# Optimization experiments

Hardware: AMD Instinct MI355X
Metric: run time of the kernel (lower is better)

The kernel has to match this reference:

```python
import jax, jax.numpy as jnp
import numpy as np

B, CIN, F, H, W = 4, 256, 128, 64, 64
EPS = 1e-5

def _conv1x1(x, Wm, b):
    # x: [B,C,H,W], Wm: [O,C] (1x1 conv kernel), b: [O]
    return jnp.einsum('bchw,oc->bohw', x, Wm) + b[None, :, None, None]

def setup_inputs() -> dict:
    key = jax.random.key(0)
    ks = jax.random.split(key, 11)
    s_in = 1.0 / np.sqrt(CIN)
    s_f = 1.0 / np.sqrt(F)
    return {
        'x':    jax.random.normal(ks[0], (B, CIN, H, W), jnp.float32),
        'Wg':   jax.random.normal(ks[1], (F, CIN), jnp.float32) * s_in,
        'bg':   jax.random.normal(ks[2], (F,), jnp.float32) * s_in,
        'Wt':   jax.random.normal(ks[3], (F, CIN), jnp.float32) * s_in,
        'bt':   jax.random.normal(ks[4], (F,), jnp.float32) * s_in,
        'Wp':   jax.random.normal(ks[5], (F, CIN), jnp.float32) * s_in,
        'bp':   jax.random.normal(ks[6], (F,), jnp.float32) * s_in,
        'Wz':   jax.random.normal(ks[7], (CIN, F), jnp.float32) * s_f,
        'bz':   jax.random.normal(ks[8], (CIN,), jnp.float32) * s_f,
        'ln_w': jax.random.normal(ks[9], (CIN, H, W), jnp.float32) * 0.1,
        'ln_b': jax.random.normal(ks[10], (CIN, H, W), jnp.float32) * 0.1,
    }

def reference(x, Wg, bg, Wt, bt, Wp, bp, Wz, bz, ln_w, ln_b):
    b, _, h, w = x.shape
    n = h * w
    # 1x1 conv projections
    g = _conv1x1(x, Wg, bg).reshape(b, F, n).transpose(0, 2, 1)      # [B,N,F]
    theta = _conv1x1(x, Wt, bt).reshape(b, F, n).transpose(0, 2, 1)  # [B,N,F]
    phi = _conv1x1(x, Wp, bp).reshape(b, F, n)                        # [B,F,N]
    # embedded-Gaussian affinity + softmax attention
    f = jnp.einsum('bnf,bfm->bnm', theta, phi)                        # [B,N,N]
    attn = jax.nn.softmax(f, axis=-1)
    y = jnp.einsum('bnm,bmf->bnf', attn, g)                           # [B,N,F]
    y = y.transpose(0, 2, 1).reshape(b, F, h, w)                      # [B,F,H,W]
    # output projection
    z = _conv1x1(y, Wz, bz)                                           # [B,CIN,H,W]
    # LayerNorm over (C,H,W) per sample, affine params shaped [C,H,W]
    mu = jnp.mean(z, axis=(1, 2, 3), keepdims=True)
    var = jnp.var(z, axis=(1, 2, 3), keepdims=True)
    z = (z - mu) * jax.lax.rsqrt(var + EPS)
    z = z * ln_w[None] + ln_b[None]
    return z + x
```

## Files before the change

kernel.cpp:

```cpp
#include <hip/hip_runtime.h>
#include <stdint.h>

#define CIN 256
#define FDIM 128
#define NSP 4096
#define EPS 1e-5f

typedef __attribute__((ext_vector_type(8))) short short8;
typedef __attribute__((ext_vector_type(4))) float f32x4;
typedef __attribute__((ext_vector_type(16))) float f32x16;

__device__ __forceinline__ short f2bf(float f) {
  union { float f; uint32_t u; } v; v.f = f;
  uint32_t r = v.u + 0x7fffu + ((v.u >> 16) & 1u);
  return (short)(r >> 16);
}
__device__ __forceinline__ float bf2f(short h) {
  union { uint32_t u; float f; } v; v.u = ((uint32_t)(uint16_t)h) << 16;
  return v.f;
}

__global__ void prep_weights(const float* __restrict__ Wg, const float* __restrict__ Wt,
                             const float* __restrict__ Wp, const float* __restrict__ Wz,
                             short* __restrict__ Wbf, short* __restrict__ Wzbf) {
  int idx = blockIdx.x * 256 + threadIdx.x;
  if (idx < 384 * 256) {
    int row = idx >> 8, col = idx & 255;
    float v;
    if (row < 128)       v = Wt[row * 256 + col];
    else if (row < 256)  v = Wp[(row - 128) * 256 + col];
    else                 v = Wg[(row - 256) * 256 + col];
    Wbf[idx] = f2bf(v);
  } else {
    int j = idx - 384 * 256;
    if (j < 256 * 128) Wzbf[j] = f2bf(Wz[j]);
  }
}

__global__ void prep_xT(const float* __restrict__ x, short* __restrict__ xT) {
  __shared__ float tile[32][33];
  int b = blockIdx.z, c0 = blockIdx.y * 32, n0 = blockIdx.x * 32;
  int r = threadIdx.x >> 5, c = threadIdx.x & 31;
  const float* xb = x + (size_t)b * CIN * NSP;
#pragma unroll
  for (int k = 0; k < 4; k++)
    tile[r + 8 * k][c] = xb[(size_t)(c0 + r + 8 * k) * NSP + n0 + c];
  __syncthreads();
  short* xTb = xT + (size_t)b * NSP * CIN;
#pragma unroll
  for (int k = 0; k < 4; k++)
    xTb[(size_t)(n0 + r + 8 * k) * CIN + c0 + c] = f2bf(tile[c][r + 8 * k]);
}

__global__ void __launch_bounds__(256)
proj_kernel(const short* __restrict__ xT, const short* __restrict__ Wbf,
            const float* __restrict__ bt, const float* __restrict__ bp,
            const float* __restrict__ bg,
            short* __restrict__ theta, short* __restrict__ Kb, short* __restrict__ gT) {
  __shared__ short lds[5120];
  int bx = blockIdx.x;
  int b = bx >> 7;
  int n0 = (bx & 127) << 5;
  int p = blockIdx.y;
  int t = threadIdx.x, w = t >> 6, lane = t & 63, l15 = lane & 15, quad = lane >> 4;

  const short* arow = xT + (size_t)(b * NSP + n0 + (w & 1) * 16 + l15) * CIN;
  short8 a[8];
#pragma unroll
  for (int s = 0; s < 8; s++) a[s] = *(const short8*)(arow + s * 32 + quad * 8);

  const short* Wsrc = Wbf + p * 128 * 256;
  f32x4 zero = {0.f, 0.f, 0.f, 0.f};
  f32x4 acc[4];
#pragma unroll
  for (int i = 0; i < 4; i++) acc[i] = zero;

#pragma unroll
  for (int s = 0; s < 8; s++) {
#pragma unroll
    for (int ft = 0; ft < 4; ft++) {
      int ftg = (w >> 1) * 4 + ft;
      short8 bfr = *(const short8*)(Wsrc + (ftg * 16 + l15) * 256 + s * 32 + quad * 8);
      acc[ft] = __builtin_amdgcn_mfma_f32_16x16x32_bf16(a[s], bfr, acc[ft], 0, 0, 0);
    }
  }

  const float* bias = (p == 0) ? bt : (p == 1) ? bp : bg;
  if (p < 2) {
#pragma unroll
    for (int ft = 0; ft < 4; ft++) {
      int ftg = (w >> 1) * 4 + ft;
      float bv = bias[ftg * 16 + l15];
#pragma unroll
      for (int rr = 0; rr < 4; rr++) {
        int n = (w & 1) * 16 + quad * 4 + rr;
        lds[n * 136 + ftg * 16 + l15] = f2bf(acc[ft][rr] + bv);
      }
    }
    __syncthreads();
    short* dst = ((p == 0) ? theta : Kb) + (size_t)(b * NSP + n0) * FDIM;
#pragma unroll
    for (int i = 0; i < 2; i++) {
      int flat = t + 256 * i;
      int row = flat >> 4, ch = flat & 15;
      *(short8*)(dst + (size_t)row * FDIM + ch * 8) = *(const short8*)(lds + row * 136 + ch * 8);
    }
  } else {
#pragma unroll
    for (int ft = 0; ft < 4; ft++) {
      int ftg = (w >> 1) * 4 + ft;
      float bv = bias[ftg * 16 + l15];
#pragma unroll
      for (int rr = 0; rr < 4; rr++) {
        int n = (w & 1) * 16 + quad * 4 + rr;
        lds[(ftg * 16 + l15) * 40 + n] = f2bf(acc[ft][rr] + bv);
      }
    }
    __syncthreads();
    short* dst = gT + (size_t)b * FDIM * NSP + n0;
#pragma unroll
    for (int i = 0; i < 2; i++) {
      int flat = t + 256 * i;
      int f = flat >> 2, c = flat & 3;
      *(short8*)(dst + (size_t)f * NSP + c * 8) = *(const short8*)(lds + f * 40 + c * 8);
    }
  }
}

__global__ void __launch_bounds__(256, 2)
flash_kernel(const short* __restrict__ thetab, const short* __restrict__ Kb,
             const short* __restrict__ gT, short* __restrict__ opart,
             float* __restrict__ lpart) {
  __shared__ __attribute__((aligned(16))) char smem[66048];
  short* KldsA = (short*)smem;
  short* KldsB = (short*)(smem + 8704);
  short* VtA   = (short*)(smem + 17408);
  short* VtB   = (short*)(smem + 27648);
  float* Om    = (float*)smem;
  float* lsm   = (float*)(smem + 65536);

  const int bx = blockIdx.x;
  const int b  = bx >> 7;
  const int r  = bx & 127;
  const int q0 = (r >> 2) << 7;
  const int kc = r & 3;
  const int t = threadIdx.x, w = t >> 6, lane = t & 63;
  const int l31 = lane & 31, h = lane >> 5;
  const int qw = q0 + (w & 1) * 64;

  const short* Qsrc = thetab + (size_t)b * NSP * FDIM;
  const short* Ksrc = Kb + (size_t)b * NSP * FDIM;
  const short* Vsrc = gT + (size_t)b * FDIM * NSP;

  short8 qf0[8], qf1[8];
#pragma unroll
  for (int s = 0; s < 8; s++) {
    qf0[s] = *(const short8*)(Qsrc + (size_t)(qw + l31) * FDIM + s * 16 + h * 8);
    qf1[s] = *(const short8*)(Qsrc + (size_t)(qw + 32 + l31) * FDIM + s * 16 + h * 8);
  }

  f32x16 O0[4], O1[4];
#pragma unroll
  for (int i = 0; i < 4; i++) {
#pragma unroll
    for (int j = 0; j < 16; j++) { O0[i][j] = 0.f; O1[i][j] = 0.f; }
  }
  float lsum0 = 0.f, lsum1 = 0.f;

  const int kA0 = kc << 10;
  for (int j0 = 0; j0 < 512; j0 += 32) {
    __syncthreads();
    int kA = kA0 + j0, kB = kA + 512;
#pragma unroll
    for (int rep = 0; rep < 2; rep++) {
      int flat = t + 256 * rep;
      int row = flat >> 4, c = flat & 15;
      *(short8*)(KldsA + row * 136 + c * 8) =
          *(const short8*)(Ksrc + (size_t)(kA + row) * FDIM + c * 8);
      *(short8*)(KldsB + row * 136 + c * 8) =
          *(const short8*)(Ksrc + (size_t)(kB + row) * FDIM + c * 8);
      int f = flat >> 2, c2 = flat & 3;
      *(short8*)(VtA + f * 40 + c2 * 8) =
          *(const short8*)(Vsrc + (size_t)f * NSP + kA + c2 * 8);
      *(short8*)(VtB + f * 40 + c2 * 8) =
          *(const short8*)(Vsrc + (size_t)f * NSP + kB + c2 * 8);
    }
    __syncthreads();
    const short* Kl = (w & 2) ? KldsB : KldsA;
    const short* Vl = (w & 2) ? VtB : VtA;

    f32x16 S0, S1;
#pragma unroll
    for (int j = 0; j < 16; j++) { S0[j] = 0.f; S1[j] = 0.f; }
#pragma unroll
    for (int s = 0; s < 8; s++) {
      short8 ak = *(const short8*)(Kl + l31 * 136 + s * 16 + h * 8);
      S0 = __builtin_amdgcn_mfma_f32_32x32x16_bf16(ak, qf0[s], S0, 0, 0, 0);
      S1 = __builtin_amdgcn_mfma_f32_32x32x16_bf16(ak, qf1[s], S1, 0, 0, 0);
    }

    short8 Af0[2], Af1[2];
#pragma unroll
    for (int qb = 0; qb < 2; qb++) {
      float p[16];
      float ls = 0.f;
#pragma unroll
      for (int i = 0; i < 16; i++) {
        p[i] = __expf(qb ? S1[i] : S0[i]);
        ls += p[i];
      }
      if (qb) lsum1 += ls; else lsum0 += ls;
#pragma unroll
      for (int tt = 0; tt < 2; tt++) {
        const int rb = tt * 8;
        short8 af;
#pragma unroll
        for (int rr = 0; rr < 4; rr++) {
          float qv = h ? p[rb + rr] : p[rb + 4 + rr];
          float wv = __shfl_xor(qv, 32, 64);
          float e0 = h ? wv : p[rb + rr];
          float e1 = h ? p[rb + 4 + rr] : wv;
          af[rr] = f2bf(e0);
          af[4 + rr] = f2bf(e1);
        }
        if (qb) Af1[tt] = af; else Af0[tt] = af;
      }
    }

#pragma unroll
    for (int ft = 0; ft < 4; ft++) {
#pragma unroll
      for (int tt = 0; tt < 2; tt++) {
        short8 bv = *(const short8*)(Vl + (ft * 32 + l31) * 40 + tt * 16 + h * 8);
        O0[ft] = __builtin_amdgcn_mfma_f32_32x32x16_bf16(Af0[tt], bv, O0[ft], 0, 0, 0);
        O1[ft] = __builtin_amdgcn_mfma_f32_32x32x16_bf16(Af1[tt], bv, O1[ft], 0, 0, 0);
      }
    }
  }

  lsum0 += __shfl_xor(lsum0, 32, 64);
  lsum1 += __shfl_xor(lsum1, 32, 64);

  __syncthreads();
  if (w >= 2) {
    float* dst = Om + (size_t)(w - 2) * 8192;
#pragma unroll
    for (int qb = 0; qb < 2; qb++) {
#pragma unroll
      for (int ft = 0; ft < 4; ft++) {
#pragma unroll
        for (int reg = 0; reg < 16; reg++) {
          int rowq = qb * 32 + (reg & 3) + 8 * (reg >> 2) + 4 * h;
          dst[rowq * 128 + ft * 32 + l31] = qb ? O1[ft][reg] : O0[ft][reg];
        }
      }
    }
    if (h == 0) {
      lsm[(w - 2) * 64 + l31] = lsum0;
      lsm[(w - 2) * 64 + 32 + l31] = lsum1;
    }
  }
  __syncthreads();
  if (w < 2) {
    const float* src = Om + (size_t)w * 8192;
    short* od = opart + ((size_t)(kc * 4 + b) * NSP + qw) * FDIM;
#pragma unroll
    for (int qb = 0; qb < 2; qb++) {
#pragma unroll
      for (int ft = 0; ft < 4; ft++) {
#pragma unroll
        for (int reg = 0; reg < 16; reg++) {
          int rowq = qb * 32 + (reg & 3) + 8 * (reg >> 2) + 4 * h;
          float v = (qb ? O1[ft][reg] : O0[ft][reg]) + src[rowq * 128 + ft * 32 + l31];
          od[(size_t)rowq * FDIM + ft * 32 + l31] = f2bf(v);
        }
      }
    }
    if (h == 0) {
      size_t lb = (size_t)(kc * 4 + b) * NSP + qw;
      lpart[lb + l31] = lsum0 + lsm[w * 64 + l31];
      lpart[lb + 32 + l31] = lsum1 + lsm[w * 64 + 32 + l31];
    }
  }
}

__global__ void __launch_bounds__(256)
zproj_kernel(const short* __restrict__ opart, const float* __restrict__ lpart,
             const short* __restrict__ Wzbf, const float* __restrict__ bz,
             short* __restrict__ zb, float* __restrict__ psums) {
  __shared__ short ldsT[128 * 40];
  __shared__ float wsum[4][2];
  int bx = blockIdx.x;
  int b = bx >> 7;
  int n0 = (bx & 127) << 5;
  int ch0 = blockIdx.y * 128;
  int t = threadIdx.x, w = t >> 6, lane = t & 63, l15 = lane & 15, quad = lane >> 4;

  int row = n0 + (w & 1) * 16 + l15;
  float L = 0.f;
#pragma unroll
  for (int kcc = 0; kcc < 4; kcc++) L += lpart[(size_t)(kcc * 4 + b) * NSP + row];
  float inv = 1.0f / L;

  short8 a[4];
#pragma unroll
  for (int s = 0; s < 4; s++) {
    float accv[8] = {0, 0, 0, 0, 0, 0, 0, 0};
#pragma unroll
    for (int kcc = 0; kcc < 4; kcc++) {
      short8 v = *(const short8*)(opart + ((size_t)(kcc * 4 + b) * NSP + row) * FDIM + s * 32 + quad * 8);
#pragma unroll
      for (int j = 0; j < 8; j++) accv[j] += bf2f(v[j]);
    }
    short8 av;
#pragma unroll
    for (int j = 0; j < 8; j++) av[j] = f2bf(accv[j] * inv);
    a[s] = av;
  }

  f32x4 zero = {0.f, 0.f, 0.f, 0.f};
  f32x4 acc[4];
#pragma unroll
  for (int i = 0; i < 4; i++) acc[i] = zero;
#pragma unroll
  for (int s = 0; s < 4; s++) {
#pragma unroll
    for (int ct = 0; ct < 4; ct++) {
      int co = ch0 + (w >> 1) * 64 + ct * 16 + l15;
      short8 bfr = *(const short8*)(Wzbf + (size_t)co * FDIM + s * 32 + quad * 8);
      acc[ct] = __builtin_amdgcn_mfma_f32_16x16x32_bf16(a[s], bfr, acc[ct], 0, 0, 0);
    }
  }

  float s1 = 0.0f, s2 = 0.0f;
#pragma unroll
  for (int ct = 0; ct < 4; ct++) {
    int cg = (w >> 1) * 64 + ct * 16 + l15;
    float bv = bz[ch0 + cg];
#pragma unroll
    for (int rr = 0; rr < 4; rr++) {
      float v = acc[ct][rr] + bv;
      s1 += v; s2 += v * v;
      ldsT[cg * 40 + (w & 1) * 16 + quad * 4 + rr] = f2bf(v);
    }
  }
#pragma unroll
  for (int off = 32; off >= 1; off >>= 1) {
    s1 += __shfl_xor(s1, off, 64);
    s2 += __shfl_xor(s2, off, 64);
  }
  if (lane == 0) { wsum[w][0] = s1; wsum[w][1] = s2; }
  __syncthreads();
  if (t == 0) {
    int bid = blockIdx.y * 512 + bx;
    psums[bid * 2] = wsum[0][0] + wsum[1][0] + wsum[2][0] + wsum[3][0];
    psums[bid * 2 + 1] = wsum[0][1] + wsum[1][1] + wsum[2][1] + wsum[3][1];
  }
  short* dst = zb + (size_t)b * CIN * NSP + (size_t)ch0 * NSP + n0;
#pragma unroll
  for (int i = 0; i < 2; i++) {
    int flat = t + 256 * i;
    int c = flat >> 2, ch = flat & 3;
    *(short8*)(dst + (size_t)c * NSP + ch * 8) = *(const short8*)(ldsT + c * 40 + ch * 8);
  }
}

__global__ void reduce_sums(const float* __restrict__ psums, float* __restrict__ sums) {
  __shared__ float red[8];
  int t = threadIdx.x;
  if (t < 8) red[t] = 0.f;
  __syncthreads();
  for (int i = t; i < 1024; i += 256) {
    int b = (i & 511) >> 7;
    atomicAdd(&red[b * 2], psums[i * 2]);
    atomicAdd(&red[b * 2 + 1], psums[i * 2 + 1]);
  }
  __syncthreads();
  if (t < 8) sums[t] = red[t];
}

__global__ void __launch_bounds__(256)
finalize_kernel(const short* __restrict__ zbuf, const float* __restrict__ x,
                const float* __restrict__ lnw, const float* __restrict__ lnb,
                const float* __restrict__ sums, float* __restrict__ out) {
  int gid = blockIdx.x * 256 + threadIdx.x;
  size_t e0 = (size_t)gid * 8;
  int b = (int)(e0 >> 20);
  size_t ib = e0 & ((size_t)(1u << 20) - 1);
  float mean = sums[b * 2] * (1.0f / 1048576.0f);
  float var = sums[b * 2 + 1] * (1.0f / 1048576.0f) - mean * mean;
  float rs = rsqrtf(var + EPS);
  short8 zv = *(const short8*)(zbuf + e0);
#pragma unroll
  for (int k = 0; k < 8; k++) {
    float z = bf2f(zv[k]);
    out[e0 + k] = (z - mean) * rs * lnw[ib + k] + lnb[ib + k] + x[e0 + k];
  }
}

extern "C" void kernel_launch(void* const* d_in, const int* in_sizes, int n_in,
                              void* d_out, int out_size, void* d_ws, size_t ws_size,
                              hipStream_t stream) {
  const float* x   = (const float*)d_in[0];
  const float* Wg  = (const float*)d_in[1];
  const float* bg  = (const float*)d_in[2];
  const float* Wt  = (const float*)d_in[3];
  const float* bt  = (const float*)d_in[4];
  const float* Wp  = (const float*)d_in[5];
  const float* bp  = (const float*)d_in[6];
  const float* Wz  = (const float*)d_in[7];
  const float* bz  = (const float*)d_in[8];
  const float* lnw = (const float*)d_in[9];
  const float* lnb = (const float*)d_in[10];
  float* out = (float*)d_out;

  char* ws = (char*)d_ws;
  short* Wbf    = (short*)(ws);
  short* Wzbf   = (short*)(ws + 196608);
  short* xT     = (short*)(ws + 262144);
  short* opart  = (short*)(ws + 262144);
  float* lpart  = (float*)(ws + 17039360);
  short* thetab = (short*)(ws + 17301504);
  short* Kb     = (short*)(ws + 21495808);
  short* gT     = (short*)(ws + 25690112);
  short* zb     = (short*)(ws + 17301504);
  float* sums   = (float*)(ws + 29884416);
  float* psums  = (float*)(ws + 29884448);

  prep_weights<<<512, 256, 0, stream>>>(Wg, Wt, Wp, Wz, Wbf, Wzbf);
  prep_xT<<<dim3(128, 8, 4), 256, 0, stream>>>(x, xT);
  proj_kernel<<<dim3(512, 3), 256, 0, stream>>>(xT, Wbf, bt, bp, bg, thetab, Kb, gT);
  flash_kernel<<<512, 256, 0, stream>>>(thetab, Kb, gT, opart, lpart);
  zproj_kernel<<<dim3(512, 2), 256, 0, stream>>>(opart, lpart, Wzbf, bz, zb, psums);
  reduce_sums<<<1, 256, 0, stream>>>(psums, sums);
  finalize_kernel<<<2048, 256, 0, stream>>>(zb, x, lnw, lnb, sums, out);
}
```

Baseline: 210.0 us.

## Double-buffer K/V tiles in LDS with register prefetch and packed bf16 conversion

The flash attention loop now double-buffers the K and V tiles in LDS. Global loads for the next tile go into registers before the PV MFMAs and are stored to the alternate buffer afterwards, which leaves one barrier per iteration instead of two and hides global latency behind compute. The P-to-bf16 conversion also now uses packed bf16x2 conversion with two shuffles of packed values instead of four float shuffles. The trade-off is more LDS (about 75KB), which may limit two blocks per CU, plus extra registers for the prefetched data.

```diff
diff --git a/kernel.cpp b/kernel.cpp
--- a/kernel.cpp
+++ b/kernel.cpp
@@ -1,4 +1,5 @@
 #include <hip/hip_runtime.h>
+#include <hip/hip_bf16.h>
 #include <stdint.h>
 
 #define CIN 256
@@ -18,6 +19,11 @@
 __device__ __forceinline__ float bf2f(short h) {
   union { uint32_t u; float f; } v; v.u = ((uint32_t)(uint16_t)h) << 16;
   return v.f;
+}
+__device__ __forceinline__ uint32_t pk2bf(float a, float b) {
+  union { __hip_bfloat162 h; uint32_t u; } cv;
+  cv.h = __float22bfloat162_rn(float2{a, b});
+  return cv.u;
 }
 
 __global__ void prep_weights(const float* __restrict__ Wg, const float* __restrict__ Wt,
@@ -131,13 +137,11 @@
 flash_kernel(const short* __restrict__ thetab, const short* __restrict__ Kb,
              const short* __restrict__ gT, short* __restrict__ opart,
              float* __restrict__ lpart) {
-  __shared__ __attribute__((aligned(16))) char smem[66048];
-  short* KldsA = (short*)smem;
-  short* KldsB = (short*)(smem + 8704);
-  short* VtA   = (short*)(smem + 17408);
-  short* VtB   = (short*)(smem + 27648);
-  float* Om    = (float*)smem;
-  float* lsm   = (float*)(smem + 65536);
+  __shared__ __attribute__((aligned(16))) char smem[75776];
+  short* Klds = (short*)smem;
+  short* Vlds = (short*)(smem + 34816);
+  float* Om   = (float*)smem;
+  float* lsm  = (float*)(smem + 65536);
 
   const int bx = blockIdx.x;
   const int b  = bx >> 7;
@@ -147,6 +151,7 @@
   const int t = threadIdx.x, w = t >> 6, lane = t & 63;
   const int l31 = lane & 31, h = lane >> 5;
   const int qw = q0 + (w & 1) * 64;
+  const int ck = w >> 1;
 
   const short* Qsrc = thetab + (size_t)b * NSP * FDIM;
   const short* Ksrc = Kb + (size_t)b * NSP * FDIM;
@@ -168,26 +173,30 @@
   float lsum0 = 0.f, lsum1 = 0.f;
 
   const int kA0 = kc << 10;
-  for (int j0 = 0; j0 < 512; j0 += 32) {
-    __syncthreads();
-    int kA = kA0 + j0, kB = kA + 512;
+
+  {
+    const int kA = kA0, kB = kA0 + 512;
 #pragma unroll
     for (int rep = 0; rep < 2; rep++) {
       int flat = t + 256 * rep;
       int row = flat >> 4, c = flat & 15;
-      *(short8*)(KldsA + row * 136 + c * 8) =
+      *(short8*)(Klds + row * 136 + c * 8) =
           *(const short8*)(Ksrc + (size_t)(kA + row) * FDIM + c * 8);
-      *(short8*)(KldsB + row * 136 + c * 8) =
+      *(short8*)(Klds + 4352 + row * 136 + c * 8) =
           *(const short8*)(Ksrc + (size_t)(kB + row) * FDIM + c * 8);
       int f = flat >> 2, c2 = flat & 3;
-      *(short8*)(VtA + f * 40 + c2 * 8) =
+      *(short8*)(Vlds + f * 40 + c2 * 8) =
           *(const short8*)(Vsrc + (size_t)f * NSP + kA + c2 * 8);
-      *(short8*)(VtB + f * 40 + c2 * 8) =
+      *(short8*)(Vlds + 5120 + f * 40 + c2 * 8) =
           *(const short8*)(Vsrc + (size_t)f * NSP + kB + c2 * 8);
     }
-    __syncthreads();
-    const short* Kl = (w & 2) ? KldsB : KldsA;
-    const short* Vl = (w & 2) ? VtB : VtA;
+  }
+  __syncthreads();
+
+  for (int it = 0; it < 16; ++it) {
+    const int cur = it & 1;
+    const short* Kl = Klds + (cur * 2 + ck) * 4352;
+    const short* Vl = Vlds + (cur * 2 + ck) * 5120;
 
     f32x16 S0, S1;
 #pragma unroll
@@ -210,20 +219,38 @@
         ls += p[i];
       }
       if (qb) lsum1 += ls; else lsum0 += ls;
+      short8* Af = qb ? Af1 : Af0;
 #pragma unroll
       for (int tt = 0; tt < 2; tt++) {
         const int rb = tt * 8;
-        short8 af;
-#pragma unroll
-        for (int rr = 0; rr < 4; rr++) {
-          float qv = h ? p[rb + rr] : p[rb + 4 + rr];
-          float wv = __shfl_xor(qv, 32, 64);
-          float e0 = h ? wv : p[rb + rr];
-          float e1 = h ? p[rb + 4 + rr] : wv;
-          af[rr] = f2bf(e0);
-          af[4 + rr] = f2bf(e1);
-        }
-        if (qb) Af1[tt] = af; else Af0[tt] = af;
+        uint32_t pk01 = pk2bf(p[rb + 0], p[rb + 1]);
+        uint32_t pk23 = pk2bf(p[rb + 2], p[rb + 3]);
+        uint32_t pk45 = pk2bf(p[rb + 4], p[rb + 5]);
+        uint32_t pk67 = pk2bf(p[rb + 6], p[rb + 7]);
+        uint32_t r0 = (uint32_t)__shfl_xor((int)(h ? pk01 : pk45), 32, 64);
+        uint32_t r1 = (uint32_t)__shfl_xor((int)(h ? pk23 : pk67), 32, 64);
+        union { uint32_t u[4]; short8 v; } u;
+        u.u[0] = h ? r0 : pk01;
+        u.u[1] = h ? r1 : pk23;
+        u.u[2] = h ? pk45 : r0;
+        u.u[3] = h ? pk67 : r1;
+        Af[tt] = u.v;
+      }
+    }
+
+    const bool more = (it + 1 < 16);
+    short8 nk0[2], nk1[2], nv0[2], nv1[2];
+    if (more) {
+      const int kA = kA0 + (it + 1) * 32, kB = kA + 512;
+#pragma unroll
+      for (int rep = 0; rep < 2; rep++) {
+        int flat = t + 256 * rep;
+        int row = flat >> 4, c = flat & 15;
+        nk0[rep] = *(const short8*)(Ksrc + (size_t)(kA + row) * FDIM + c * 8);
+        nk1[rep] = *(const short8*)(Ksrc + (size_t)(kB + row) * FDIM + c * 8);
+        int f = flat >> 2, c2 = flat & 3;
+        nv0[rep] = *(const short8*)(Vsrc + (size_t)f * NSP + kA + c2 * 8);
+        nv1[rep] = *(const short8*)(Vsrc + (size_t)f * NSP + kB + c2 * 8);
       }
     }
 
@@ -235,6 +262,22 @@
         O0[ft] = __builtin_amdgcn_mfma_f32_32x32x16_bf16(Af0[tt], bv, O0[ft], 0, 0, 0);
         O1[ft] = __builtin_amdgcn_mfma_f32_32x32x16_bf16(Af1[tt], bv, O1[ft], 0, 0, 0);
       }
+    }
+
+    if (more) {
+      short* Kd = Klds + ((it + 1) & 1) * 2 * 4352;
+      short* Vd = Vlds + ((it + 1) & 1) * 2 * 5120;
+#pragma unroll
+      for (int rep = 0; rep < 2; rep++) {
+        int flat = t + 256 * rep;
+        int row = flat >> 4, c = flat & 15;
+        *(short8*)(Kd + row * 136 + c * 8) = nk0[rep];
+        *(short8*)(Kd + 4352 + row * 136 + c * 8) = nk1[rep];
+        int f = flat >> 2, c2 = flat & 3;
+        *(short8*)(Vd + f * 40 + c2 * 8) = nv0[rep];
+        *(short8*)(Vd + 5120 + f * 40 + c2 * 8) = nv1[rep];
+      }
+      __syncthreads();
     }
   }
 
```

Result: no change. 210.4 us (+0.2%).
